# Optimization experiments

Measured on AMD Instinct MI355X. Metric: run time of the kernel, lower is better.

## Reference

```python
import jax, jax.numpy as jnp
import numpy as np

EPS = 1e-6

def setup_inputs() -> dict:
    key = jax.random.key(0)
    k1, k2 = jax.random.split(key)
    b, seq, d = 4, 512, 64
    x = jax.random.normal(k1, (b, seq, d, d), dtype=jnp.float32)
    # diagonal decay rates in (0, 1): realistic SSM decay, positive like the clamped param
    A = jax.random.uniform(k2, (d,), dtype=jnp.float32)
    return {"x": x, "A": A}

def reference(x, A):
    b, seq, d, _ = x.shape
    log_A = jnp.log(jnp.clip(A, EPS))                      # (d,)
    # cumsum over seq of the (constant-in-time) log decay, as in the original
    cs_A = jnp.cumsum(jnp.broadcast_to(log_A, (seq, d)), axis=0)  # (seq, d)
    log_M = cs_A[:, None, :] - cs_A[None, :, :]            # (t, j, d)
    idx = jnp.arange(seq)
    mask = idx[:, None] >= idx[None, :]                    # causal: t >= j
    M = jnp.where(mask[:, :, None], jnp.exp(log_M), 0.0)   # (t, j, d)
    # A is batch-independent, so M is shared across batch (same math as the original)
    out = jnp.einsum('tjr,bjrc->btrc', M, x)               # (b, seq, d, d)
    return out
```

## Files before the change

### kernel.cpp

```cpp
#include <hip/hip_runtime.h>


#define B_   4
#define SEQ_ 512
#define D_   64
#define CHUNK_ 32
#define NWAVE_ (SEQ_ / CHUNK_)

__global__ __launch_bounds__(NWAVE_ * 64) void ssm_scan_kernel(
    const float* __restrict__ x, const float* __restrict__ A,
    float* __restrict__ out)
{
    __shared__ float Elds[NWAVE_ * D_];

    const int blk = blockIdx.x;
    const int bi  = blk >> 6;
    const int r   = blk & 63;
    const int tid = threadIdx.x;
    const int w   = tid >> 6;
    const int c   = tid & 63;

    const float a = fmaxf(A[r], 1e-6f);

    const int j0 = w * CHUNK_;
    const size_t base = ((size_t)(bi * SEQ_ + j0) * D_ + r) * D_ + c;
    const float* xp = x + base;
    float*       op = out + base;
    const int jstride = D_ * D_;

    float local[CHUNK_];
    float state = 0.0f;
    #pragma unroll
    for (int t = 0; t < CHUNK_; ++t) {
        float v = xp[(size_t)t * jstride];
        state = fmaf(state, a, v);
        local[t] = state;
    }

    Elds[w * D_ + c] = state;
    __syncthreads();

    float aL = a * a;
    aL = aL * aL;
    aL = aL * aL;
    aL = aL * aL;
    aL = aL * aL;

    float carry = 0.0f;
    for (int wp = 0; wp < w; ++wp) {
        carry = fmaf(carry, aL, Elds[wp * D_ + c]);
    }

    float p = a;
    #pragma unroll
    for (int t = 0; t < CHUNK_; ++t) {
        op[(size_t)t * jstride] = fmaf(carry, p, local[t]);
        p *= a;
    }
}

extern "C" void kernel_launch(void* const* d_in, const int* in_sizes, int n_in,
                              void* d_out, int out_size, void* d_ws, size_t ws_size,
                              hipStream_t stream) {
    const float* x   = (const float*)d_in[0];
    const float* A   = (const float*)d_in[1];
    float*       out = (float*)d_out;

    dim3 grid(B_ * D_);
    dim3 block(NWAVE_ * 64);
    hipLaunchKernelGGL(ssm_scan_kernel, grid, block, 0, stream, x, A, out);
}
```

Before: 82.86 us.

## Vectorize columns as float4 and shrink sequence chunks to raise scan parallelism

Each thread now handles four adjacent columns through float4 loads and stores, and sequence chunks shrink from 32 to 8 steps, giving 64 chunks per block with the same 1024 threads. This aims for wider memory transactions and a shorter serial dependency chain per thread. The price is a longer carry loop over up to 63 previous chunk totals read from shared memory, with the decay power recomputed as a^8.

```diff
diff --git a/kernel.cpp b/kernel.cpp
--- a/kernel.cpp
+++ b/kernel.cpp
@@ -1,60 +1,71 @@
 #include <hip/hip_runtime.h>
 
 
-#define B_   4
-#define SEQ_ 512
-#define D_   64
-#define CHUNK_ 32
-#define NWAVE_ (SEQ_ / CHUNK_)
+#define B_    4
+#define SEQ_  512
+#define D_    64
+#define CH_   8
+#define NCH_  (SEQ_ / CH_)
+#define NCQ_  (D_ / 4)
+#define NTHR_ (NCH_ * NCQ_)
 
-__global__ __launch_bounds__(NWAVE_ * 64) void ssm_scan_kernel(
+__global__ __launch_bounds__(NTHR_) void ssm_scan_kernel(
     const float* __restrict__ x, const float* __restrict__ A,
     float* __restrict__ out)
 {
-    __shared__ float Elds[NWAVE_ * D_];
+    __shared__ float4 Elds[NCH_][NCQ_];
 
     const int blk = blockIdx.x;
     const int bi  = blk >> 6;
     const int r   = blk & 63;
     const int tid = threadIdx.x;
-    const int w   = tid >> 6;
-    const int c   = tid & 63;
+    const int ch  = tid >> 4;
+    const int cq  = tid & 15;
 
     const float a = fmaxf(A[r], 1e-6f);
 
-    const int j0 = w * CHUNK_;
-    const size_t base = ((size_t)(bi * SEQ_ + j0) * D_ + r) * D_ + c;
-    const float* xp = x + base;
-    float*       op = out + base;
-    const int jstride = D_ * D_;
+    const int j0 = ch * CH_;
+    const size_t base = ((size_t)(bi * SEQ_ + j0) * D_ + r) * D_ + cq * 4;
+    const float4* xp = (const float4*)(x + base);
+    float4*       op = (float4*)(out + base);
+    const int jstride4 = (D_ * D_) / 4;
 
-    float local[CHUNK_];
-    float state = 0.0f;
+    float4 loc[CH_];
+    float s0 = 0.f, s1 = 0.f, s2 = 0.f, s3 = 0.f;
     #pragma unroll
-    for (int t = 0; t < CHUNK_; ++t) {
-        float v = xp[(size_t)t * jstride];
-        state = fmaf(state, a, v);
-        local[t] = state;
+    for (int t = 0; t < CH_; ++t) {
+        float4 v = xp[(size_t)t * jstride4];
+        s0 = fmaf(s0, a, v.x);
+        s1 = fmaf(s1, a, v.y);
+        s2 = fmaf(s2, a, v.z);
+        s3 = fmaf(s3, a, v.w);
+        loc[t] = make_float4(s0, s1, s2, s3);
     }
 
-    Elds[w * D_ + c] = state;
+    Elds[ch][cq] = make_float4(s0, s1, s2, s3);
     __syncthreads();
 
-    float aL = a * a;
-    aL = aL * aL;
-    aL = aL * aL;
-    aL = aL * aL;
-    aL = aL * aL;
+    float a2 = a * a, a4 = a2 * a2, aL = a4 * a4;
 
-    float carry = 0.0f;
-    for (int wp = 0; wp < w; ++wp) {
-        carry = fmaf(carry, aL, Elds[wp * D_ + c]);
+    float c0 = 0.f, c1 = 0.f, c2 = 0.f, c3 = 0.f;
+    for (int cp = 0; cp < ch; ++cp) {
+        float4 e = Elds[cp][cq];
+        c0 = fmaf(c0, aL, e.x);
+        c1 = fmaf(c1, aL, e.y);
+        c2 = fmaf(c2, aL, e.z);
+        c3 = fmaf(c3, aL, e.w);
     }
 
     float p = a;
     #pragma unroll
-    for (int t = 0; t < CHUNK_; ++t) {
-        op[(size_t)t * jstride] = fmaf(carry, p, local[t]);
+    for (int t = 0; t < CH_; ++t) {
+        float4 l = loc[t];
+        float4 o;
+        o.x = fmaf(c0, p, l.x);
+        o.y = fmaf(c1, p, l.y);
+        o.z = fmaf(c2, p, l.z);
+        o.w = fmaf(c3, p, l.w);
+        op[(size_t)t * jstride4] = o;
         p *= a;
     }
 }
@@ -67,6 +78,6 @@
     float*       out = (float*)d_out;
 
     dim3 grid(B_ * D_);
-    dim3 block(NWAVE_ * 64);
+    dim3 block(NTHR_);
     hipLaunchKernelGGL(ssm_scan_kernel, grid, block, 0, stream, x, A, out);
 }
```

Measured after the change: 82.58 us. No clear change (-0.3%).
